# Optimization experiments

Measured on AMD Instinct MI355X. Metric: run time of the kernel, lower is better.

## Reference

```python
import jax, jax.numpy as jnp
import numpy as np

N = 8_388_608
T_MAX = 4096


def setup_inputs() -> dict:
    key = jax.random.key(0)
    k1, k2, k3 = jax.random.split(key, 3)
    risk = jax.random.normal(k1, (N,), dtype=jnp.float32)
    time = jax.random.randint(k2, (N,), 0, T_MAX, dtype=jnp.int64)
    event = jax.random.randint(k3, (N,), 0, 2, dtype=jnp.int64)
    return {"risk": risk, "time": time, "event": event}


def reference(risk, time, event):
    # Sort descending by time (matches torch.argsort(time, descending=True)).
    order = jnp.argsort(-time)
    r = risk[order]            # [N] risk sorted by descending time
    t = time[order]            # [N]
    e = event[order] > 0       # [N] bool

    n = r.shape[0]
    # Cumulative (prefix) logsumexp over descending-sorted risks.
    # At-risk set for time t is exactly the prefix ending at the LAST index
    # of t's tie group, so log_denom(group) = clse[last_idx_of_group].
    clse = jax.lax.associative_scan(jnp.logaddexp, r)  # [N]

    # Last index of each contiguous tie block (times equal => contiguous after sort).
    is_last = jnp.concatenate([t[:-1] != t[1:], jnp.ones((1,), dtype=bool)])
    idx = jnp.arange(n)
    cand = jnp.where(is_last, idx, n)          # non-last positions -> sentinel
    last_idx = jax.lax.cummin(cand, axis=0, reverse=True)  # min over j >= i

    log_denom = clse[last_idx]                 # [N] per-sample group denominator

    # nll = -sum_groups(sum_{events in group} risk  -  d_group * log_denom)
    #     =  sum_{i: event_i} (log_denom_i - risk_i)
    nll = jnp.sum(jnp.where(e, log_denom - r, jnp.float32(0.0)))

    has_events = jnp.sum(event > 0) > 0
    return jnp.where(has_events, nll, jnp.float32(0.0))
```

## Files before the change

kernel.cpp:

```cpp
#include <hip/hip_runtime.h>

#define TMAX 4096
#define ABLOCKS 512
#define ATHREADS 1024
#define PERTHREAD_V4 4

#define SCALE_F 1048576.0f
#define INV_SCALE (1.0 / 1048576.0)
#define SUM_MASK 0xFFFFFFFFFFFFULL
#define CNT_SHIFT 48

#define RB 64
#define RS 16

#define PROC1(rv, tv, ev)                                                     \
    {                                                                         \
        const unsigned pk32 = (unsigned)(__expf(rv) * SCALE_F + 0.5f);        \
        const unsigned long long pk = (unsigned long long)pk32                \
            | ((unsigned long long)(unsigned)(ev) << CNT_SHIFT);              \
        atomicAdd(&s_acc[(tv) & (TMAX - 1)], pk);                             \
        evr = __builtin_fmaf((float)(ev), (rv), evr);                        \
    }

#define PROC4(rr, tt, ee)                                                     \
    PROC1((rr).x, (tt).x, (ee).x)                                             \
    PROC1((rr).y, (tt).y, (ee).y)                                             \
    PROC1((rr).z, (tt).z, (ee).z)                                             \
    PROC1((rr).w, (tt).w, (ee).w)

__global__ __launch_bounds__(ATHREADS, 8) void coxph_hist_fixed(
    const float* __restrict__ risk, const int* __restrict__ time_,
    const int* __restrict__ event,
    unsigned long long* __restrict__ pacc, float* __restrict__ pevr)
{
    __shared__ unsigned long long s_acc[TMAX];
    __shared__ float s_evr[ATHREADS / 64];

    const int tid = threadIdx.x;
    #pragma unroll
    for (int k = 0; k < TMAX / ATHREADS; ++k) s_acc[tid + k * ATHREADS] = 0ull;
    __syncthreads();

    const float4* r4 = (const float4*)risk;
    const int4*   t4 = (const int4*)time_;
    const int4*   e4 = (const int4*)event;

    const int base = blockIdx.x * ATHREADS + tid;
    const int S4   = ABLOCKS * ATHREADS;

    float evr = 0.f;

    float4 r0 = r4[base];          int4 t0 = t4[base];          int4 e0 = e4[base];
    float4 r1 = r4[base + S4];     int4 t1 = t4[base + S4];     int4 e1 = e4[base + S4];

    float4 r2 = r4[base + 2 * S4]; int4 t2 = t4[base + 2 * S4]; int4 e2 = e4[base + 2 * S4];
    PROC4(r0, t0, e0)

    float4 r3 = r4[base + 3 * S4]; int4 t3 = t4[base + 3 * S4]; int4 e3 = e4[base + 3 * S4];
    PROC4(r1, t1, e1)

    PROC4(r2, t2, e2)
    PROC4(r3, t3, e3)

    #pragma unroll
    for (int off = 32; off > 0; off >>= 1) evr += __shfl_down(evr, off);
    const int lane = tid & 63, wave = tid >> 6;
    if (lane == 0) s_evr[wave] = evr;
    __syncthreads();

    unsigned long long* pa = pacc + (size_t)blockIdx.x * TMAX;
    #pragma unroll
    for (int k = 0; k < TMAX / ATHREADS; ++k) {
        const int i = tid + k * ATHREADS;
        pa[i] = s_acc[i];
    }
    if (tid == 0) {
        float tot = 0.f;
        for (int w = 0; w < ATHREADS / 64; ++w) tot += s_evr[w];
        pevr[blockIdx.x] = tot;
    }
}

__global__ __launch_bounds__(ATHREADS, 8) void coxph_hist_generic(
    const float* __restrict__ risk, const int* __restrict__ time_,
    const int* __restrict__ event,
    unsigned long long* __restrict__ pacc, float* __restrict__ pevr, int n)
{
    __shared__ unsigned long long s_acc[TMAX];
    __shared__ float s_evr[ATHREADS / 64];

    const int tid = threadIdx.x;
    #pragma unroll
    for (int k = 0; k < TMAX / ATHREADS; ++k) s_acc[tid + k * ATHREADS] = 0ull;
    __syncthreads();

    float evr = 0.f;
    const int stride = gridDim.x * ATHREADS;
    for (int i = blockIdx.x * ATHREADS + tid; i < n; i += stride) {
        float rv = risk[i];
        int   ev = event[i];
        int   tv = time_[i];
        PROC1(rv, tv, ev)
    }

    #pragma unroll
    for (int off = 32; off > 0; off >>= 1) evr += __shfl_down(evr, off);
    const int lane = tid & 63, wave = tid >> 6;
    if (lane == 0) s_evr[wave] = evr;
    __syncthreads();

    unsigned long long* pa = pacc + (size_t)blockIdx.x * TMAX;
    #pragma unroll
    for (int k = 0; k < TMAX / ATHREADS; ++k) {
        const int i = tid + k * ATHREADS;
        pa[i] = s_acc[i];
    }
    if (tid == 0) {
        float tot = 0.f;
        for (int w = 0; w < ATHREADS / 64; ++w) tot += s_evr[w];
        pevr[blockIdx.x] = tot;
    }
}

__global__ __launch_bounds__(1024) void coxph_reduce(
    const unsigned long long* __restrict__ pacc,
    unsigned long long* __restrict__ gaccR)
{
    __shared__ unsigned long long ls[RS * RB];

    const int t = threadIdx.x;
    const int j = t & (RB - 1);
    const int s = t >> 6;
    const int bucket = blockIdx.x * RB + j;

    unsigned long long sum = 0ull;
    #pragma unroll
    for (int k = 0; k < ABLOCKS / RS; ++k) {
        const int row = s * (ABLOCKS / RS) + k;
        sum += pacc[(size_t)row * TMAX + bucket];
    }
    ls[t] = sum;
    __syncthreads();

    #pragma unroll
    for (int h = RS / 2; h >= 1; h >>= 1) {
        if (s < h) ls[t] += ls[t + h * RB];
        __syncthreads();
    }
    if (s == 0) gaccR[TMAX - 1 - bucket] = ls[j];
}

__global__ __launch_bounds__(1024) void coxph_finalize(
    const unsigned long long* __restrict__ gaccR,
    const float* __restrict__ pevr, int nevr, float* __restrict__ out)
{
    __shared__ float    s_wsum[16];
    __shared__ double   s_dacc[16];
    __shared__ unsigned s_cacc[16];

    const int tid = threadIdx.x;
    const int lane = tid & 63, wave = tid >> 6;

    const ulonglong4 g = ((const ulonglong4*)gaccR)[tid];
    const float v0 = (float)((double)(g.x & SUM_MASK) * INV_SCALE);
    const float v1 = (float)((double)(g.y & SUM_MASK) * INV_SCALE);
    const float v2 = (float)((double)(g.z & SUM_MASK) * INV_SCALE);
    const float v3 = (float)((double)(g.w & SUM_MASK) * INV_SCALE);
    const unsigned c0 = (unsigned)(g.x >> CNT_SHIFT);
    const unsigned c1 = (unsigned)(g.y >> CNT_SHIFT);
    const unsigned c2 = (unsigned)(g.z >> CNT_SHIFT);
    const unsigned c3 = (unsigned)(g.w >> CNT_SHIFT);

    const float p0 = v0, p1 = p0 + v1, p2 = p1 + v2, p3 = p2 + v3;

    float t_incl = p3;
    #pragma unroll
    for (int off = 1; off < 64; off <<= 1) {
        float u = __shfl_up(t_incl, off);
        if (lane >= off) t_incl += u;
    }
    if (lane == 63) s_wsum[wave] = t_incl;
    __syncthreads();
    if (tid == 0) {
        float a = 0.f;
        for (int w = 0; w < 16; ++w) { float x = s_wsum[w]; s_wsum[w] = a; a += x; }
    }
    __syncthreads();
    const float excl = (t_incl - p3) + s_wsum[wave];

    double acc = 0.0; unsigned ctot = 0u;
    if (c0) { acc += (double)c0 * (double)logf(excl + p0); ctot += c0; }
    if (c1) { acc += (double)c1 * (double)logf(excl + p1); ctot += c1; }
    if (c2) { acc += (double)c2 * (double)logf(excl + p2); ctot += c2; }
    if (c3) { acc += (double)c3 * (double)logf(excl + p3); ctot += c3; }

    if (tid < nevr) acc -= (double)pevr[tid];

    #pragma unroll
    for (int off = 32; off > 0; off >>= 1) {
        acc  += __shfl_down(acc, off);
        ctot += __shfl_down(ctot, off);
    }
    if (lane == 0) { s_dacc[wave] = acc; s_cacc[wave] = ctot; }
    __syncthreads();
    if (tid == 0) {
        double a = 0.0; unsigned cc = 0u;
        for (int w = 0; w < 16; ++w) { a += s_dacc[w]; cc += s_cacc[w]; }
        out[0] = cc ? (float)a : 0.0f;
    }
}

extern "C" void kernel_launch(void* const* d_in, const int* in_sizes, int n_in,
                              void* d_out, int out_size, void* d_ws, size_t ws_size,
                              hipStream_t stream)
{
    const float* risk  = (const float*)d_in[0];
    const int*   time_ = (const int*)d_in[1];
    const int*   event = (const int*)d_in[2];
    float* out = (float*)d_out;
    const int n = in_sizes[0];

    char* ws = (char*)d_ws;
    size_t off = 0;
    unsigned long long* pacc  = (unsigned long long*)(ws + off);
    off += (size_t)ABLOCKS * TMAX * sizeof(unsigned long long);
    float*              pevr  = (float*)(ws + off);
    off += ABLOCKS * sizeof(float);
    unsigned long long* gaccR = (unsigned long long*)(ws + off);
    off += TMAX * sizeof(unsigned long long);

    if (n == ABLOCKS * ATHREADS * 4 * PERTHREAD_V4) {
        coxph_hist_fixed<<<ABLOCKS, ATHREADS, 0, stream>>>(
            risk, time_, event, pacc, pevr);
    } else {
        coxph_hist_generic<<<ABLOCKS, ATHREADS, 0, stream>>>(
            risk, time_, event, pacc, pevr, n);
    }
    coxph_reduce<<<TMAX / RB, RS * RB, 0, stream>>>(pacc, gaccR);
    coxph_finalize<<<1, 1024, 0, stream>>>(gaccR, pevr, ABLOCKS, out);
}
```

Measured before the change: 129.6 us.

## Replace per-block partial histograms and reduce kernel with global atomics

Each histogram block now merges its shared-memory bins straight into one global histogram using 64-bit atomics, with zero bins skipped. This removes the separate reduction kernel and the large per-block partial buffer write and read. The grid is halved to 256 blocks, each thread handles 8 vectors, and loads are software-pipelined. A memset is added, and contention on the global atomics grows with block count.

```diff
diff --git a/kernel.cpp b/kernel.cpp
--- a/kernel.cpp
+++ b/kernel.cpp
@@ -1,37 +1,36 @@
 #include <hip/hip_runtime.h>
 
 #define TMAX 4096
-#define ABLOCKS 512
+#define ABLOCKS 256
 #define ATHREADS 1024
-#define PERTHREAD_V4 4
+#define PERTHREAD_V4 8
 
 #define SCALE_F 1048576.0f
 #define INV_SCALE (1.0 / 1048576.0)
 #define SUM_MASK 0xFFFFFFFFFFFFULL
 #define CNT_SHIFT 48
 
-#define RB 64
-#define RS 16
-
 #define PROC1(rv, tv, ev)                                                     \
-    {                                                                         \
+    do {                                                                      \
         const unsigned pk32 = (unsigned)(__expf(rv) * SCALE_F + 0.5f);        \
         const unsigned long long pk = (unsigned long long)pk32                \
             | ((unsigned long long)(unsigned)(ev) << CNT_SHIFT);              \
         atomicAdd(&s_acc[(tv) & (TMAX - 1)], pk);                             \
-        evr = __builtin_fmaf((float)(ev), (rv), evr);                        \
-    }
+        evr = __builtin_fmaf((float)(ev), (rv), evr);                         \
+    } while (0)
 
 #define PROC4(rr, tt, ee)                                                     \
-    PROC1((rr).x, (tt).x, (ee).x)                                             \
-    PROC1((rr).y, (tt).y, (ee).y)                                             \
-    PROC1((rr).z, (tt).z, (ee).z)                                             \
-    PROC1((rr).w, (tt).w, (ee).w)
-
-__global__ __launch_bounds__(ATHREADS, 8) void coxph_hist_fixed(
+    do {                                                                      \
+        PROC1((rr).x, (tt).x, (ee).x);                                        \
+        PROC1((rr).y, (tt).y, (ee).y);                                        \
+        PROC1((rr).z, (tt).z, (ee).z);                                        \
+        PROC1((rr).w, (tt).w, (ee).w);                                        \
+    } while (0)
+
+__global__ __launch_bounds__(ATHREADS, 4) void coxph_hist_fixed(
     const float* __restrict__ risk, const int* __restrict__ time_,
     const int* __restrict__ event,
-    unsigned long long* __restrict__ pacc, float* __restrict__ pevr)
+    unsigned long long* __restrict__ gaccR, float* __restrict__ pevr)
 {
     __shared__ unsigned long long s_acc[TMAX];
     __shared__ float s_evr[ATHREADS / 64];
@@ -50,17 +49,23 @@
 
     float evr = 0.f;
 
-    float4 r0 = r4[base];          int4 t0 = t4[base];          int4 e0 = e4[base];
-    float4 r1 = r4[base + S4];     int4 t1 = t4[base + S4];     int4 e1 = e4[base + S4];
-
-    float4 r2 = r4[base + 2 * S4]; int4 t2 = t4[base + 2 * S4]; int4 e2 = e4[base + 2 * S4];
-    PROC4(r0, t0, e0)
-
-    float4 r3 = r4[base + 3 * S4]; int4 t3 = t4[base + 3 * S4]; int4 e3 = e4[base + 3 * S4];
-    PROC4(r1, t1, e1)
-
-    PROC4(r2, t2, e2)
-    PROC4(r3, t3, e3)
+    float4 r[PERTHREAD_V4]; int4 t[PERTHREAD_V4]; int4 e[PERTHREAD_V4];
+
+    #pragma unroll
+    for (int k = 0; k < 4; ++k) {
+        const int i = base + k * S4;
+        r[k] = r4[i]; t[k] = t4[i]; e[k] = e4[i];
+    }
+    #pragma unroll
+    for (int k = 0; k < 4; ++k) {
+        const int i = base + (k + 4) * S4;
+        r[k + 4] = r4[i]; t[k + 4] = t4[i]; e[k + 4] = e4[i];
+        PROC4(r[k], t[k], e[k]);
+    }
+    #pragma unroll
+    for (int k = 4; k < 8; ++k) {
+        PROC4(r[k], t[k], e[k]);
+    }
 
     #pragma unroll
     for (int off = 32; off > 0; off >>= 1) evr += __shfl_down(evr, off);
@@ -68,11 +73,11 @@
     if (lane == 0) s_evr[wave] = evr;
     __syncthreads();
 
-    unsigned long long* pa = pacc + (size_t)blockIdx.x * TMAX;
     #pragma unroll
     for (int k = 0; k < TMAX / ATHREADS; ++k) {
         const int i = tid + k * ATHREADS;
-        pa[i] = s_acc[i];
+        const unsigned long long v = s_acc[i];
+        if (v) atomicAdd(&gaccR[TMAX - 1 - i], v);
     }
     if (tid == 0) {
         float tot = 0.f;
@@ -81,10 +86,10 @@
     }
 }
 
-__global__ __launch_bounds__(ATHREADS, 8) void coxph_hist_generic(
+__global__ __launch_bounds__(ATHREADS, 4) void coxph_hist_generic(
     const float* __restrict__ risk, const int* __restrict__ time_,
     const int* __restrict__ event,
-    unsigned long long* __restrict__ pacc, float* __restrict__ pevr, int n)
+    unsigned long long* __restrict__ gaccR, float* __restrict__ pevr, int n)
 {
     __shared__ unsigned long long s_acc[TMAX];
     __shared__ float s_evr[ATHREADS / 64];
@@ -100,7 +105,7 @@
         float rv = risk[i];
         int   ev = event[i];
         int   tv = time_[i];
-        PROC1(rv, tv, ev)
+        PROC1(rv, tv, ev);
     }
 
     #pragma unroll
@@ -109,45 +114,17 @@
     if (lane == 0) s_evr[wave] = evr;
     __syncthreads();
 
-    unsigned long long* pa = pacc + (size_t)blockIdx.x * TMAX;
     #pragma unroll
     for (int k = 0; k < TMAX / ATHREADS; ++k) {
         const int i = tid + k * ATHREADS;
-        pa[i] = s_acc[i];
+        const unsigned long long v = s_acc[i];
+        if (v) atomicAdd(&gaccR[TMAX - 1 - i], v);
     }
     if (tid == 0) {
         float tot = 0.f;
         for (int w = 0; w < ATHREADS / 64; ++w) tot += s_evr[w];
         pevr[blockIdx.x] = tot;
     }
-}
-
-__global__ __launch_bounds__(1024) void coxph_reduce(
-    const unsigned long long* __restrict__ pacc,
-    unsigned long long* __restrict__ gaccR)
-{
-    __shared__ unsigned long long ls[RS * RB];
-
-    const int t = threadIdx.x;
-    const int j = t & (RB - 1);
-    const int s = t >> 6;
-    const int bucket = blockIdx.x * RB + j;
-
-    unsigned long long sum = 0ull;
-    #pragma unroll
-    for (int k = 0; k < ABLOCKS / RS; ++k) {
-        const int row = s * (ABLOCKS / RS) + k;
-        sum += pacc[(size_t)row * TMAX + bucket];
-    }
-    ls[t] = sum;
-    __syncthreads();
-
-    #pragma unroll
-    for (int h = RS / 2; h >= 1; h >>= 1) {
-        if (s < h) ls[t] += ls[t + h * RB];
-        __syncthreads();
-    }
-    if (s == 0) gaccR[TMAX - 1 - bucket] = ls[j];
 }
 
 __global__ __launch_bounds__(1024) void coxph_finalize(
@@ -222,20 +199,19 @@
 
     char* ws = (char*)d_ws;
     size_t off = 0;
-    unsigned long long* pacc  = (unsigned long long*)(ws + off);
-    off += (size_t)ABLOCKS * TMAX * sizeof(unsigned long long);
+    unsigned long long* gaccR = (unsigned long long*)(ws + off);
+    off += TMAX * sizeof(unsigned long long);
     float*              pevr  = (float*)(ws + off);
     off += ABLOCKS * sizeof(float);
-    unsigned long long* gaccR = (unsigned long long*)(ws + off);
-    off += TMAX * sizeof(unsigned long long);
+
+    (void)hipMemsetAsync(gaccR, 0, TMAX * sizeof(unsigned long long), stream);
 
     if (n == ABLOCKS * ATHREADS * 4 * PERTHREAD_V4) {
         coxph_hist_fixed<<<ABLOCKS, ATHREADS, 0, stream>>>(
-            risk, time_, event, pacc, pevr);
+            risk, time_, event, gaccR, pevr);
     } else {
         coxph_hist_generic<<<ABLOCKS, ATHREADS, 0, stream>>>(
-            risk, time_, event, pacc, pevr, n);
-    }
-    coxph_reduce<<<TMAX / RB, RS * RB, 0, stream>>>(pacc, gaccR);
+            risk, time_, event, gaccR, pevr, n);
+    }
     coxph_finalize<<<1, 1024, 0, stream>>>(gaccR, pevr, ABLOCKS, out);
 }
```

Measured after the change: 122.8 us. 5.3% less time.
